# Kernel tuning notes

Hardware: AMD Instinct MI355X
Metric: run time of the kernel (lower is better)

## Reference

```python
import jax, jax.numpy as jnp
import numpy as np

H = 4            # attention heads
N = 50000        # num nodes
E = 800000       # num edges
IN, HID, OUT = 256, 32, 32
NEG_SLOPE = 0.2  # DGL GATConv default leaky_relu slope


def setup_inputs() -> dict:
    key = jax.random.key(0)
    ks = jax.random.split(key, 16)
    x = jax.random.normal(ks[0], (N, IN), jnp.float32)
    src = jax.random.randint(ks[1], (E,), 0, N, dtype=jnp.int32)
    dst = jax.random.randint(ks[2], (E,), 0, N, dtype=jnp.int32)

    def lin(k, a, b):
        return jax.random.normal(k, (a, b), jnp.float32) * (1.0 / np.sqrt(a))

    def attn(k, d):
        return jax.random.normal(k, (H, d), jnp.float32) * 0.1

    HW = H * HID
    return {
        "x": x, "src": src, "dst": dst,
        "W1": lin(ks[3], IN, HW), "al1": attn(ks[4], HID), "ar1": attn(ks[5], HID), "b1": jnp.zeros((H, HID), jnp.float32),
        "W2": lin(ks[6], HW, HW), "al2": attn(ks[7], HID), "ar2": attn(ks[8], HID), "b2": jnp.zeros((H, HID), jnp.float32),
        "W3": lin(ks[9], HW, H * OUT), "al3": attn(ks[10], OUT), "ar3": attn(ks[11], OUT), "b3": jnp.zeros((H, OUT), jnp.float32),
    }


def gat_layer(x, W, al, ar, b, src, dst, act):
    # x: [N, F_in]; W: [F_in, H*D]; al/ar/b: [H, D]
    n = x.shape[0]
    d = al.shape[1]
    h = (x @ W).reshape(n, H, d)                         # [N, H, D]
    el = jnp.sum(h * al, axis=-1)                        # [N, H]
    er = jnp.sum(h * ar, axis=-1)                        # [N, H]
    e = jax.nn.leaky_relu(el[src] + er[dst], NEG_SLOPE)  # [E, H] edge scores
    # segment softmax over incoming edges of each dst node
    m = jax.ops.segment_max(e, dst, num_segments=n)      # [N, H]
    m = jnp.where(jnp.isfinite(m), m, 0.0)               # empty segments -> -inf
    ex = jnp.exp(e - m[dst])                             # [E, H]
    s = jax.ops.segment_sum(ex, dst, num_segments=n)     # [N, H]
    alpha = ex / s[dst]                                  # [E, H]
    out = jax.ops.segment_sum(h[src] * alpha[:, :, None], dst, num_segments=n)  # [N, H, D]
    out = out + b
    return act(out) if act is not None else out


def reference(x, src, dst, W1, al1, ar1, b1, W2, al2, ar2, b2, W3, al3, ar3, b3):
    h = gat_layer(x, W1, al1, ar1, b1, src, dst, jax.nn.relu).reshape(N, -1)   # flatten heads
    h = gat_layer(h, W2, al2, ar2, b2, src, dst, jax.nn.elu).reshape(N, -1)    # flatten heads
    h = gat_layer(h, W3, al3, ar3, b3, src, dst, None).mean(axis=1)            # mean over heads
    return h
```

## Files before the change

kernel.cpp:

```cpp
#include <hip/hip_runtime.h>
#include <hip/hip_bf16.h>
#include <stdint.h>

#define NNODES 50000
#define NEDGES 800000
#define HEADS 4
#define DSTRIDE 64

#define GEMM_GRID ((NNODES + 127) / 128)
#define B2_GROUPS 8
#define B2_PER_GROUP 256
#define NODES_PER_GROUP (NNODES / B2_GROUPS)

typedef __attribute__((ext_vector_type(8))) short bf16x8;
typedef __attribute__((ext_vector_type(4))) float f32x4;

union frag_u { uint32_t u[4]; bf16x8 v; uint4 q; };

__device__ __forceinline__ float lrelu(float x) { return x > 0.f ? x : 0.2f * x; }

__device__ __forceinline__ uint32_t pack_bf16(float a, float b) {
  __hip_bfloat162 t{__float2bfloat16(a), __float2bfloat16(b)};
  return *reinterpret_cast<uint32_t*>(&t);
}

__device__ __forceinline__ void split8(const float4& x0, const float4& x1,
                                       frag_u& hi, frag_u& lo) {
  float f[8] = {x0.x, x0.y, x0.z, x0.w, x1.x, x1.y, x1.z, x1.w};
#pragma unroll
  for (int p = 0; p < 4; ++p) {
    uint32_t ua = __float_as_uint(f[2 * p]);
    uint32_t ub = __float_as_uint(f[2 * p + 1]);
    hi.u[p] = (ua >> 16) | (ub & 0xffff0000u);
    float ra = f[2 * p] - __uint_as_float(ua & 0xffff0000u);
    float rb = f[2 * p + 1] - __uint_as_float(ub & 0xffff0000u);
    lo.u[p] = (__float_as_uint(ra) >> 16) | (__float_as_uint(rb) & 0xffff0000u);
  }
}

__global__ __launch_bounds__(256) void k_build2(const int* __restrict__ src,
                                                const int* __restrict__ dst,
                                                int* __restrict__ cnt,
                                                int* __restrict__ esrc) {
  int g = blockIdx.x & (B2_GROUPS - 1);
  int sub = blockIdx.x >> 3;
  int lo = g * NODES_PER_GROUP, hi = lo + NODES_PER_GROUP;
  const int stride = B2_PER_GROUP * 256;
  for (int e = sub * 256 + threadIdx.x; e < NEDGES; e += stride) {
    int d = dst[e];
    if (d >= lo && d < hi) {
      int r = atomicAdd(&cnt[d], 1);
      if (r < DSTRIDE) esrc[(size_t)d * DSTRIDE + r] = src[e];
    }
  }
}

__device__ __forceinline__ void splitw_one(const float* __restrict__ W, int t_local,
                                           uint4* __restrict__ WPh, uint4* __restrict__ WPl) {
  int lane = t_local & 63;
  int ct = (t_local >> 6) & 7;
  int ks = t_local >> 9;
  int lg = lane >> 4, lm = lane & 15;
  int n = ct * 16 + lm;
  frag_u hi, lo;
#pragma unroll
  for (int p = 0; p < 4; ++p) {
    float a = W[(size_t)(ks * 32 + lg * 8 + 2 * p) * 128 + n];
    float b = W[(size_t)(ks * 32 + lg * 8 + 2 * p + 1) * 128 + n];
    uint32_t ua = __float_as_uint(a), ub = __float_as_uint(b);
    hi.u[p] = (ua >> 16) | (ub & 0xffff0000u);
    float ra = a - __uint_as_float(ua & 0xffff0000u);
    float rb = b - __uint_as_float(ub & 0xffff0000u);
    lo.u[p] = (__float_as_uint(ra) >> 16) | (__float_as_uint(rb) & 0xffff0000u);
  }
  WPh[t_local] = hi.q;
  WPl[t_local] = lo.q;
}

__global__ void k_splitw_all(const float* __restrict__ W1, const float* __restrict__ W2,
                             const float* __restrict__ W3,
                             uint4* __restrict__ WPh1, uint4* __restrict__ WPl1,
                             uint4* __restrict__ WPh2, uint4* __restrict__ WPl2,
                             uint4* __restrict__ WPh3, uint4* __restrict__ WPl3) {
  int t = blockIdx.x * blockDim.x + threadIdx.x;
  int ks = t >> 9;
  if (ks < 8)        splitw_one(W1, t,            WPh1, WPl1);
  else if (ks < 12)  splitw_one(W2, t - 8 * 512,  WPh2, WPl2);
  else if (ks < 16)  splitw_one(W3, t - 12 * 512, WPh3, WPl3);
}

template <int K>
__global__ __launch_bounds__(256) void k_gemm_mfma(
    const float* __restrict__ X, const uint4* __restrict__ WPh,
    const uint4* __restrict__ WPl, const float* __restrict__ al,
    const float* __restrict__ ar, uint32_t* __restrict__ Hb,
    float* __restrict__ el, float* __restrict__ er, int nrows) {
  const int tid = threadIdx.x;
  const int wv = tid >> 6;
  const int lane = tid & 63;
  const int lm = lane & 15;
  const int lg = lane >> 4;
  const int rbase = blockIdx.x * 128 + wv * 32;

  int grow0 = rbase + lm;
  int grow1 = rbase + 16 + lm;
  int lrow0 = min(grow0, nrows - 1);
  int lrow1 = min(grow1, nrows - 1);
  const float* xp0 = X + (size_t)lrow0 * K + lg * 8;
  const float* xp1 = X + (size_t)lrow1 * K + lg * 8;

  f32x4 acc[2][8];
#pragma unroll
  for (int rt = 0; rt < 2; ++rt)
#pragma unroll
    for (int ct = 0; ct < 8; ++ct) acc[rt][ct] = f32x4{0.f, 0.f, 0.f, 0.f};

  for (int ks = 0; ks < K / 32; ++ks) {
    float4 a0 = *(const float4*)(xp0 + ks * 32);
    float4 a1 = *(const float4*)(xp0 + ks * 32 + 4);
    float4 b0 = *(const float4*)(xp1 + ks * 32);
    float4 b1 = *(const float4*)(xp1 + ks * 32 + 4);
    frag_u xh0, xl0, xh1, xl1;
    split8(a0, a1, xh0, xl0);
    split8(b0, b1, xh1, xl1);
    const uint4* wph = WPh + (size_t)(ks * 8) * 64 + lane;
    const uint4* wpl = WPl + (size_t)(ks * 8) * 64 + lane;
#pragma unroll
    for (int ct = 0; ct < 8; ++ct) {
      frag_u bh, bl;
      bh.q = wph[ct * 64];
      bl.q = wpl[ct * 64];
      acc[0][ct] = __builtin_amdgcn_mfma_f32_16x16x32_bf16(bh.v, xh0.v, acc[0][ct], 0, 0, 0);
      acc[0][ct] = __builtin_amdgcn_mfma_f32_16x16x32_bf16(bl.v, xh0.v, acc[0][ct], 0, 0, 0);
      acc[0][ct] = __builtin_amdgcn_mfma_f32_16x16x32_bf16(bh.v, xl0.v, acc[0][ct], 0, 0, 0);
      acc[1][ct] = __builtin_amdgcn_mfma_f32_16x16x32_bf16(bh.v, xh1.v, acc[1][ct], 0, 0, 0);
      acc[1][ct] = __builtin_amdgcn_mfma_f32_16x16x32_bf16(bl.v, xh1.v, acc[1][ct], 0, 0, 0);
      acc[1][ct] = __builtin_amdgcn_mfma_f32_16x16x32_bf16(bh.v, xl1.v, acc[1][ct], 0, 0, 0);
    }
  }

#pragma unroll
  for (int rt = 0; rt < 2; ++rt) {
    int grow = rt ? grow1 : grow0;
    float pe[4] = {0.f, 0.f, 0.f, 0.f};
    float pr[4] = {0.f, 0.f, 0.f, 0.f};
#pragma unroll
    for (int ct = 0; ct < 8; ++ct) {
      int h = ct >> 1;
      int dc = (ct & 1) * 16 + lg * 4;
      float4 a4 = *(const float4*)&al[h * 32 + dc];
      float4 r4 = *(const float4*)&ar[h * 32 + dc];
      f32x4 c = acc[rt][ct];
      pe[h] += c[0] * a4.x + c[1] * a4.y + c[2] * a4.z + c[3] * a4.w;
      pr[h] += c[0] * r4.x + c[1] * r4.y + c[2] * r4.z + c[3] * r4.w;
    }
#pragma unroll
    for (int i = 0; i < 4; ++i) {
      pe[i] += __shfl_xor(pe[i], 16); pe[i] += __shfl_xor(pe[i], 32);
      pr[i] += __shfl_xor(pr[i], 16); pr[i] += __shfl_xor(pr[i], 32);
    }
    if (grow < nrows) {
#pragma unroll
      for (int ct = 0; ct < 8; ++ct) {
        f32x4 c = acc[rt][ct];
        uint2 st{pack_bf16(c[0], c[1]), pack_bf16(c[2], c[3])};
        *(uint2*)&Hb[(size_t)grow * 64 + ct * 8 + lg * 2] = st;
      }
      if (lg == 0) {
        *(float4*)&el[(size_t)grow * 4] = float4{pe[0], pe[1], pe[2], pe[3]};
        *(float4*)&er[(size_t)grow * 4] = float4{pr[0], pr[1], pr[2], pr[3]};
      }
    }
  }
}

template <int MODE>
__global__ __launch_bounds__(256) void k_agg(const uint32_t* __restrict__ Hb,
                                             const float* __restrict__ el,
                                             const float* __restrict__ er,
                                             const int* __restrict__ deg_,
                                             const int* __restrict__ esrc,
                                             const float* __restrict__ B,
                                             float* __restrict__ out) {
  int gt = blockIdx.x * blockDim.x + threadIdx.x;
  int v = gt >> 6;
  int lane = gt & 63;
  if (v >= NNODES) return;
  int deg = min(deg_[v], DSTRIDE);
  int h = lane >> 4;
  int e16 = lane & 15;
  float erh = er[(size_t)v * 4 + h];
  const int vbase = v * DSTRIDE;

  float den = 0.f, acc0 = 0.f, acc1 = 0.f;
  for (int base = 0; base < deg; base += 16) {
    int u = 0;
    float ex1 = 0.f;
    if (base + e16 < deg) {
      u = esrc[vbase + base + e16];
      float e = el[(size_t)u * 4 + h] + erh;
      ex1 = __expf(lrelu(e));
      den += ex1;
    }
    uint32_t hw[16];
    float w[16];
#pragma unroll
    for (int j = 0; j < 16; ++j) {
      int srcl = (lane & 48) | j;
      int uj = __shfl(u, srcl);
      w[j] = __shfl(ex1, srcl);
      hw[j] = Hb[(size_t)uj * 64 + lane];
    }
#pragma unroll
    for (int j = 0; j < 16; ++j) {
      acc0 += w[j] * __uint_as_float(hw[j] << 16);
      acc1 += w[j] * __uint_as_float(hw[j] & 0xffff0000u);
    }
  }
#pragma unroll
  for (int s = 1; s < 16; s <<= 1) den += __shfl_xor(den, s);
  float inv = den > 0.f ? 1.f / den : 0.f;

  int d = (2 * lane) & 31;
  float v0 = acc0 * inv + B[h * 32 + d];
  float v1 = acc1 * inv + B[h * 32 + d + 1];

  if (MODE == 0) {
    float2 o{fmaxf(v0, 0.f), fmaxf(v1, 0.f)};
    *(float2*)(out + (size_t)v * 128 + 2 * lane) = o;
  } else if (MODE == 1) {
    float2 o{v0 > 0.f ? v0 : expm1f(v0), v1 > 0.f ? v1 : expm1f(v1)};
    *(float2*)(out + (size_t)v * 128 + 2 * lane) = o;
  } else {
    float t0 = v0, t1 = v1;
    t0 += __shfl_xor(t0, 16); t0 += __shfl_xor(t0, 32);
    t1 += __shfl_xor(t1, 16); t1 += __shfl_xor(t1, 32);
    if (lane < 16) {
      float2 o{t0 * 0.25f, t1 * 0.25f};
      *(float2*)(out + (size_t)v * 32 + 2 * lane) = o;
    }
  }
}

extern "C" void kernel_launch(void* const* d_in, const int* in_sizes, int n_in,
                              void* d_out, int out_size, void* d_ws, size_t ws_size,
                              hipStream_t stream) {
  const float* x   = (const float*)d_in[0];
  const int* src   = (const int*)d_in[1];
  const int* dst   = (const int*)d_in[2];
  const float* W1  = (const float*)d_in[3];
  const float* al1 = (const float*)d_in[4];
  const float* ar1 = (const float*)d_in[5];
  const float* b1  = (const float*)d_in[6];
  const float* W2  = (const float*)d_in[7];
  const float* al2 = (const float*)d_in[8];
  const float* ar2 = (const float*)d_in[9];
  const float* b2  = (const float*)d_in[10];
  const float* W3  = (const float*)d_in[11];
  const float* al3 = (const float*)d_in[12];
  const float* ar3 = (const float*)d_in[13];
  const float* b3  = (const float*)d_in[14];

  uint8_t* p = (uint8_t*)d_ws;
  auto alloc = [&](size_t bytes) {
    uint8_t* r = p;
    p += (bytes + 255) & ~(size_t)255;
    return r;
  };
  float* Abuf     = (float*)alloc((size_t)NNODES * 128 * 4);
  uint32_t* Hb    = (uint32_t*)alloc((size_t)NNODES * 64 * 4);
  float* el       = (float*)alloc((size_t)NNODES * 4 * 4);
  float* er       = (float*)alloc((size_t)NNODES * 4 * 4);
  int* cnt        = (int*)alloc((size_t)NNODES * 4);
  int* esrc       = (int*)alloc((size_t)NNODES * DSTRIDE * 4);
  uint4* WPh1     = (uint4*)alloc((size_t)256 * 16 * 16);
  uint4* WPl1     = (uint4*)alloc((size_t)256 * 16 * 16);
  uint4* WPh2     = (uint4*)alloc((size_t)128 * 16 * 16);
  uint4* WPl2     = (uint4*)alloc((size_t)128 * 16 * 16);
  uint4* WPh3     = (uint4*)alloc((size_t)128 * 16 * 16);
  uint4* WPl3     = (uint4*)alloc((size_t)128 * 16 * 16);

  hipMemsetAsync(cnt, 0, (size_t)NNODES * 4, stream);
  k_splitw_all<<<32, 256, 0, stream>>>(W1, W2, W3, WPh1, WPl1, WPh2, WPl2, WPh3, WPl3);
  k_build2<<<B2_GROUPS * B2_PER_GROUP, 256, 0, stream>>>(src, dst, cnt, esrc);

  const int agg_grid = (NNODES * 64 + 255) / 256;

  k_gemm_mfma<256><<<GEMM_GRID, 256, 0, stream>>>(x, WPh1, WPl1, al1, ar1, Hb, el, er, NNODES);
  k_agg<0><<<agg_grid, 256, 0, stream>>>(Hb, el, er, cnt, esrc, b1, Abuf);

  k_gemm_mfma<128><<<GEMM_GRID, 256, 0, stream>>>(Abuf, WPh2, WPl2, al2, ar2, Hb, el, er, NNODES);
  k_agg<1><<<agg_grid, 256, 0, stream>>>(Hb, el, er, cnt, esrc, b2, Abuf);

  k_gemm_mfma<128><<<GEMM_GRID, 256, 0, stream>>>(Abuf, WPh3, WPl3, al3, ar3, Hb, el, er, NNODES);
  k_agg<2><<<agg_grid, 256, 0, stream>>>(Hb, el, er, cnt, esrc, b3, (float*)d_out);
}
```

Baseline: 236.4 us.

## Halve GEMM rows per wave and pack source index with fp16 weight in shuffles

The projection GEMM now gives each wave one 16-row tile instead of two. This cuts accumulator registers and doubles the grid, trading less reuse of each loaded weight fragment for higher occupancy. In the aggregation loop, the source node index (16 bits) and the edge exp weight (as fp16) are packed into one 32-bit value, halving the cross-lane shuffles per edge. The risks are reduced precision in edge weights, a mismatch with the fp32 denominator, possible fp16 overflow for large scores, and a hard limit of 65536 nodes.

```diff
diff --git a/kernel.cpp b/kernel.cpp
--- a/kernel.cpp
+++ b/kernel.cpp
@@ -1,5 +1,6 @@
 #include <hip/hip_runtime.h>
 #include <hip/hip_bf16.h>
+#include <hip/hip_fp16.h>
 #include <stdint.h>
 
 #define NNODES 50000
@@ -7,7 +8,7 @@
 #define HEADS 4
 #define DSTRIDE 64
 
-#define GEMM_GRID ((NNODES + 127) / 128)
+#define GEMM_GRID ((NNODES + 63) / 64)
 #define B2_GROUPS 8
 #define B2_PER_GROUP 256
 #define NODES_PER_GROUP (NNODES / B2_GROUPS)
@@ -100,29 +101,20 @@
   const int lane = tid & 63;
   const int lm = lane & 15;
   const int lg = lane >> 4;
-  const int rbase = blockIdx.x * 128 + wv * 32;
-
-  int grow0 = rbase + lm;
-  int grow1 = rbase + 16 + lm;
-  int lrow0 = min(grow0, nrows - 1);
-  int lrow1 = min(grow1, nrows - 1);
-  const float* xp0 = X + (size_t)lrow0 * K + lg * 8;
-  const float* xp1 = X + (size_t)lrow1 * K + lg * 8;
-
-  f32x4 acc[2][8];
-#pragma unroll
-  for (int rt = 0; rt < 2; ++rt)
-#pragma unroll
-    for (int ct = 0; ct < 8; ++ct) acc[rt][ct] = f32x4{0.f, 0.f, 0.f, 0.f};
+
+  int grow = blockIdx.x * 64 + wv * 16 + lm;
+  int lrow = min(grow, nrows - 1);
+  const float* xp = X + (size_t)lrow * K + lg * 8;
+
+  f32x4 acc[8];
+#pragma unroll
+  for (int ct = 0; ct < 8; ++ct) acc[ct] = f32x4{0.f, 0.f, 0.f, 0.f};
 
   for (int ks = 0; ks < K / 32; ++ks) {
-    float4 a0 = *(const float4*)(xp0 + ks * 32);
-    float4 a1 = *(const float4*)(xp0 + ks * 32 + 4);
-    float4 b0 = *(const float4*)(xp1 + ks * 32);
-    float4 b1 = *(const float4*)(xp1 + ks * 32 + 4);
-    frag_u xh0, xl0, xh1, xl1;
-    split8(a0, a1, xh0, xl0);
-    split8(b0, b1, xh1, xl1);
+    float4 a0 = *(const float4*)(xp + ks * 32);
+    float4 a1 = *(const float4*)(xp + ks * 32 + 4);
+    frag_u xh, xl;
+    split8(a0, a1, xh, xl);
     const uint4* wph = WPh + (size_t)(ks * 8) * 64 + lane;
     const uint4* wpl = WPl + (size_t)(ks * 8) * 64 + lane;
 #pragma unroll
@@ -130,46 +122,39 @@
       frag_u bh, bl;
       bh.q = wph[ct * 64];
       bl.q = wpl[ct * 64];
-      acc[0][ct] = __builtin_amdgcn_mfma_f32_16x16x32_bf16(bh.v, xh0.v, acc[0][ct], 0, 0, 0);
-      acc[0][ct] = __builtin_amdgcn_mfma_f32_16x16x32_bf16(bl.v, xh0.v, acc[0][ct], 0, 0, 0);
-      acc[0][ct] = __builtin_amdgcn_mfma_f32_16x16x32_bf16(bh.v, xl0.v, acc[0][ct], 0, 0, 0);
-      acc[1][ct] = __builtin_amdgcn_mfma_f32_16x16x32_bf16(bh.v, xh1.v, acc[1][ct], 0, 0, 0);
-      acc[1][ct] = __builtin_amdgcn_mfma_f32_16x16x32_bf16(bl.v, xh1.v, acc[1][ct], 0, 0, 0);
-      acc[1][ct] = __builtin_amdgcn_mfma_f32_16x16x32_bf16(bh.v, xl1.v, acc[1][ct], 0, 0, 0);
-    }
-  }
-
-#pragma unroll
-  for (int rt = 0; rt < 2; ++rt) {
-    int grow = rt ? grow1 : grow0;
-    float pe[4] = {0.f, 0.f, 0.f, 0.f};
-    float pr[4] = {0.f, 0.f, 0.f, 0.f};
+      acc[ct] = __builtin_amdgcn_mfma_f32_16x16x32_bf16(bh.v, xh.v, acc[ct], 0, 0, 0);
+      acc[ct] = __builtin_amdgcn_mfma_f32_16x16x32_bf16(bl.v, xh.v, acc[ct], 0, 0, 0);
+      acc[ct] = __builtin_amdgcn_mfma_f32_16x16x32_bf16(bh.v, xl.v, acc[ct], 0, 0, 0);
+    }
+  }
+
+  float pe[4] = {0.f, 0.f, 0.f, 0.f};
+  float pr[4] = {0.f, 0.f, 0.f, 0.f};
+#pragma unroll
+  for (int ct = 0; ct < 8; ++ct) {
+    int h = ct >> 1;
+    int dc = (ct & 1) * 16 + lg * 4;
+    float4 a4 = *(const float4*)&al[h * 32 + dc];
+    float4 r4 = *(const float4*)&ar[h * 32 + dc];
+    f32x4 c = acc[ct];
+    pe[h] += c[0] * a4.x + c[1] * a4.y + c[2] * a4.z + c[3] * a4.w;
+    pr[h] += c[0] * r4.x + c[1] * r4.y + c[2] * r4.z + c[3] * r4.w;
+  }
+#pragma unroll
+  for (int i = 0; i < 4; ++i) {
+    pe[i] += __shfl_xor(pe[i], 16); pe[i] += __shfl_xor(pe[i], 32);
+    pr[i] += __shfl_xor(pr[i], 16); pr[i] += __shfl_xor(pr[i], 32);
+  }
+  if (grow < nrows) {
 #pragma unroll
     for (int ct = 0; ct < 8; ++ct) {
-      int h = ct >> 1;
-      int dc = (ct & 1) * 16 + lg * 4;
-      float4 a4 = *(const float4*)&al[h * 32 + dc];
-      float4 r4 = *(const float4*)&ar[h * 32 + dc];
-      f32x4 c = acc[rt][ct];
-      pe[h] += c[0] * a4.x + c[1] * a4.y + c[2] * a4.z + c[3] * a4.w;
-      pr[h] += c[0] * r4.x + c[1] * r4.y + c[2] * r4.z + c[3] * r4.w;
-    }
-#pragma unroll
-    for (int i = 0; i < 4; ++i) {
-      pe[i] += __shfl_xor(pe[i], 16); pe[i] += __shfl_xor(pe[i], 32);
-      pr[i] += __shfl_xor(pr[i], 16); pr[i] += __shfl_xor(pr[i], 32);
-    }
-    if (grow < nrows) {
-#pragma unroll
-      for (int ct = 0; ct < 8; ++ct) {
-        f32x4 c = acc[rt][ct];
-        uint2 st{pack_bf16(c[0], c[1]), pack_bf16(c[2], c[3])};
-        *(uint2*)&Hb[(size_t)grow * 64 + ct * 8 + lg * 2] = st;
-      }
-      if (lg == 0) {
-        *(float4*)&el[(size_t)grow * 4] = float4{pe[0], pe[1], pe[2], pe[3]};
-        *(float4*)&er[(size_t)grow * 4] = float4{pr[0], pr[1], pr[2], pr[3]};
-      }
+      f32x4 c = acc[ct];
+      uint2 st{pack_bf16(c[0], c[1]), pack_bf16(c[2], c[3])};
+      *(uint2*)&Hb[(size_t)grow * 64 + ct * 8 + lg * 2] = st;
+    }
+    if (lg == 0) {
+      *(float4*)&el[(size_t)grow * 4] = float4{pe[0], pe[1], pe[2], pe[3]};
+      *(float4*)&er[(size_t)grow * 4] = float4{pr[0], pr[1], pr[2], pr[3]};
     }
   }
 }
@@ -194,22 +179,21 @@
 
   float den = 0.f, acc0 = 0.f, acc1 = 0.f;
   for (int base = 0; base < deg; base += 16) {
-    int u = 0;
-    float ex1 = 0.f;
+    uint32_t pk = 0;
     if (base + e16 < deg) {
-      u = esrc[vbase + base + e16];
-      float e = el[(size_t)u * 4 + h] + erh;
-      ex1 = __expf(lrelu(e));
+      int u = esrc[vbase + base + e16];
+      float ex1 = __expf(lrelu(el[(size_t)u * 4 + h] + erh));
       den += ex1;
+      pk = ((uint32_t)u << 16) | (uint32_t)__half_as_ushort(__float2half(ex1));
     }
     uint32_t hw[16];
     float w[16];
 #pragma unroll
     for (int j = 0; j < 16; ++j) {
       int srcl = (lane & 48) | j;
-      int uj = __shfl(u, srcl);
-      w[j] = __shfl(ex1, srcl);
-      hw[j] = Hb[(size_t)uj * 64 + lane];
+      uint32_t pkj = __shfl(pk, srcl);
+      w[j] = __half2float(__ushort_as_half((unsigned short)(pkj & 0xffffu)));
+      hw[j] = Hb[(size_t)(pkj >> 16) * 64 + lane];
     }
 #pragma unroll
     for (int j = 0; j < 16; ++j) {
```

Result: faster. 230.6 us (-2.5%).
